# Kernel tuning notes

Hardware: AMD Instinct MI355X
Metric: run time of the kernel (lower is better)

The kernel has to match this reference:

```python
import jax, jax.numpy as jnp
import numpy as np

NEG_INF = jnp.float32(-9e15)

def gat_layer(x, adj_mask, W, a, alpha):
    # x: [N, F_in]; W: [H, F_in, F_out]; a: [H, 2*F_out]; adj_mask: [N, N] bool
    H, _, O = W.shape
    h = jnp.einsum('nf,hfo->hno', x, W)            # [H, N, O]
    a_src, a_dst = a[:, :O], a[:, O:]              # [H, O] each
    e_src = jnp.einsum('hno,ho->hn', h, a_src)     # [H, N]
    e_dst = jnp.einsum('hno,ho->hn', h, a_dst)     # [H, N]
    e = jax.nn.leaky_relu(e_src[:, :, None] + e_dst[:, None, :], negative_slope=alpha)
    e = jnp.where(adj_mask[None, :, :], e, NEG_INF)  # mask non-edges
    attn = jax.nn.softmax(e, axis=-1)              # [H, N, N]
    out = jnp.einsum('hnm,hmo->hno', attn, h)      # [H, N, O]
    return out.mean(axis=0)                        # average heads -> [N, O]

def setup_inputs() -> dict:
    key = jax.random.key(0)
    ks = jax.random.split(key, 6)
    N, F_IN, F_HID, F_CLS, H = 4096, 512, 256, 16, 4
    x = jax.random.normal(ks[0], (N, F_IN), dtype=jnp.float32)
    adj = jax.random.randint(ks[1], (N, N), 0, 2, dtype=jnp.int32)
    W1 = jax.random.normal(ks[2], (H, F_IN, F_HID), dtype=jnp.float32) * 0.05
    a1 = jax.random.normal(ks[3], (H, 2 * F_HID), dtype=jnp.float32) * 0.05
    W2 = jax.random.normal(ks[4], (1, F_HID, F_CLS), dtype=jnp.float32) * 0.05
    a2 = jax.random.normal(ks[5], (1, 2 * F_CLS), dtype=jnp.float32) * 0.05
    return {"x": x, "adj": adj, "W1": W1, "a1": a1, "W2": W2, "a2": a2}

def reference(x, adj, W1, a1, W2, a2):
    alpha = 0.2
    adj_mask = adj > 0
    h = jax.nn.relu(gat_layer(x, adj_mask, W1, a1, alpha))        # layer1 + ReLU
    out = gat_layer(h, adj_mask, W2, a2, alpha)                    # layer2
    return jax.nn.log_softmax(out, axis=1)                         # [N, nclass]
```

## Files before the change

### kernel.cpp

```cpp
#include <hip/hip_runtime.h>
#include <stdint.h>

#define N_NODES 4096
#define F_IN    512
#define F_HID   256
#define F_CLS   16
#define NHEAD   4
#define ALPHA   0.2f
#define LOG2E   1.4426950408889634f

typedef __attribute__((ext_vector_type(8))) short short8;
typedef __attribute__((ext_vector_type(4))) float f32x4;

__device__ __forceinline__ float bf2f(unsigned short h) {
    unsigned u = ((unsigned)h) << 16; float f; __builtin_memcpy(&f, &u, 4); return f;
}
__device__ __forceinline__ unsigned short f2bf(float f) {
    unsigned u; __builtin_memcpy(&u, &f, 4);
    u += 0x7fffu + ((u >> 16) & 1u);
    return (unsigned short)(u >> 16);
}
__device__ __forceinline__ float lo_bf(unsigned u) { u <<= 16;          float f; __builtin_memcpy(&f,&u,4); return f; }
__device__ __forceinline__ float hi_bf(unsigned u) { u &= 0xffff0000u;  float f; __builtin_memcpy(&f,&u,4); return f; }

__device__ __forceinline__ void async_cp16(void* lds, const void* g) {
    __builtin_amdgcn_global_load_lds(
        (const __attribute__((address_space(1))) unsigned int*)g,
        (__attribute__((address_space(3))) unsigned int*)lds,
        16, 0, 0);
}

__device__ __forceinline__ void pipe_barrier_vm2() {
    __builtin_amdgcn_sched_barrier(0);
    __builtin_amdgcn_s_waitcnt(0x0072);
    __builtin_amdgcn_s_barrier();
    __builtin_amdgcn_sched_barrier(0);
}
__device__ __forceinline__ void pipe_barrier_vm3() {
    __builtin_amdgcn_sched_barrier(0);
    __builtin_amdgcn_s_waitcnt(0x0073);
    __builtin_amdgcn_s_barrier();
    __builtin_amdgcn_sched_barrier(0);
}

#define PREP_BM_BLOCKS   16384
#define PREP_CV_BLOCKS   1296
#define PREP_Z_BLOCKS    4
__global__ __launch_bounds__(256) void k_prep(const int* __restrict__ adj,
                                              const float* __restrict__ x,
                                              const float* __restrict__ W1,
                                              const float* __restrict__ W2,
                                              unsigned long long* __restrict__ bm,
                                              unsigned short* __restrict__ xb,
                                              unsigned short* __restrict__ W1t,
                                              float* __restrict__ W2t,
                                              float* __restrict__ ez) {
    int b = blockIdx.x;
    if (b < PREP_BM_BLOCKS) {
        int wv = threadIdx.x >> 6, lane = threadIdx.x & 63;
        int idx0 = b * 1024 + wv * 256;
        const int* p = adj + idx0 + lane;
        unsigned long long m0 = __ballot(p[0]   > 0);
        unsigned long long m1 = __ballot(p[64]  > 0);
        unsigned long long m2 = __ballot(p[128] > 0);
        unsigned long long m3 = __ballot(p[192] > 0);
        if (lane == 0) {
            int w = idx0 >> 6;
            bm[w] = m0; bm[w+1] = m1; bm[w+2] = m2; bm[w+3] = m3;
        }
        return;
    }
    if (b < PREP_BM_BLOCKS + PREP_CV_BLOCKS) {
        int tid = (b - PREP_BM_BLOCKS) * 256 + threadIdx.x;
        const int NXV = (N_NODES * F_IN) / 8;
        const int NW1 = NHEAD * 64 * F_HID;
        if (tid < NXV) {
            float4 a = *(const float4*)&x[tid * 8];
            float4 c = *(const float4*)&x[tid * 8 + 4];
            uint4 w;
            w.x = (unsigned)f2bf(a.x) | ((unsigned)f2bf(a.y) << 16);
            w.y = (unsigned)f2bf(a.z) | ((unsigned)f2bf(a.w) << 16);
            w.z = (unsigned)f2bf(c.x) | ((unsigned)f2bf(c.y) << 16);
            w.w = (unsigned)f2bf(c.z) | ((unsigned)f2bf(c.w) << 16);
            *(uint4*)&xb[tid * 8] = w;
        } else if (tid < NXV + NW1) {
            int j = tid - NXV;
            int o = j & 255, f8 = (j >> 8) & 63, h = j >> 14;
            float v[8];
            #pragma unroll
            for (int k = 0; k < 8; ++k)
                v[k] = W1[(size_t)(h * F_IN + f8 * 8 + k) * F_HID + o];
            uint4 w;
            w.x = (unsigned)f2bf(v[0]) | ((unsigned)f2bf(v[1]) << 16);
            w.y = (unsigned)f2bf(v[2]) | ((unsigned)f2bf(v[3]) << 16);
            w.z = (unsigned)f2bf(v[4]) | ((unsigned)f2bf(v[5]) << 16);
            w.w = (unsigned)f2bf(v[6]) | ((unsigned)f2bf(v[7]) << 16);
            *(uint4*)&W1t[(size_t)(h * F_HID + o) * F_IN + f8 * 8] = w;
        } else {
            int j = tid - NXV - NW1;
            if (j < F_HID * F_CLS) {
                int o = j >> 4, c = j & 15;
                W2t[c * F_HID + o] = W2[j];
            }
        }
        return;
    }
    {
        int zb = b - PREP_BM_BLOCKS - PREP_CV_BLOCKS;
        float4* z4 = (float4*)ez;
        #pragma unroll
        for (int r = 0; r < 8; ++r)
            z4[zb * 2048 + r * 256 + threadIdx.x] = make_float4(0.f, 0.f, 0.f, 0.f);
    }
}

__global__ __launch_bounds__(256, 4) void k_gemm1(const unsigned short* __restrict__ xb,
                                                  const unsigned short* __restrict__ W1t,
                                                  const float* __restrict__ a1,
                                                  unsigned short* __restrict__ h1t,
                                                  float* __restrict__ es1,
                                                  float* __restrict__ ed1) {
    __shared__ unsigned short Sld[3][6144];
    const int t = threadIdx.x;
    const int lane = t & 63, wv = t >> 6, quad = lane >> 4, l15 = lane & 15;
    const int wn = wv & 1, wo = wv >> 1;
    const int n0 = blockIdx.x * 128;
    const int oo0 = blockIdx.y * 64;
    const int h = blockIdx.z;
    const int kl = (lane >> 4) * 8;

    const unsigned short* gs[3];
    int loff[3];
    #pragma unroll
    for (int s = 0; s < 3; ++s) {
        int c = wv * 3 + s;
        loff[s] = c * 512;
        gs[s] = (c < 8)
            ? (xb  + (size_t)(n0 + c * 16 + l15) * F_IN + kl)
            : (W1t + (size_t)(h * F_HID + oo0 + (c - 8) * 16 + l15) * F_IN + kl);
    }
    #pragma unroll
    for (int s = 0; s < 3; ++s) async_cp16(&Sld[0][loff[s]], gs[s]);
    #pragma unroll
    for (int s = 0; s < 3; ++s) async_cp16(&Sld[1][loff[s]], gs[s] + 32);

    f32x4 acc[4][2] = {};
    int cur = 0;
    for (int it = 0; it < 16; ++it) {
        pipe_barrier_vm3();
        {
            const int nxt = (cur >= 1) ? cur - 1 : 2;
            const int off = ((it + 2) & 15) * 32;
            #pragma unroll
            for (int s = 0; s < 3; ++s) async_cp16(&Sld[nxt][loff[s]], gs[s] + off);
        }
        short8 bfw[2];
        #pragma unroll
        for (int mi = 0; mi < 2; ++mi)
            bfw[mi] = *(const short8*)&Sld[cur][(8 + wo * 2 + mi) * 512 + lane * 8];
        #pragma unroll
        for (int ni = 0; ni < 4; ++ni) {
            short8 af = *(const short8*)&Sld[cur][(wn * 4 + ni) * 512 + lane * 8];
            #pragma unroll
            for (int mi = 0; mi < 2; ++mi)
                acc[ni][mi] = __builtin_amdgcn_mfma_f32_16x16x32_bf16(af, bfw[mi], acc[ni][mi], 0, 0, 0);
        }
        cur = (cur == 2) ? 0 : cur + 1;
    }
    #pragma unroll
    for (int ni = 0; ni < 4; ++ni)
      #pragma unroll
      for (int mi = 0; mi < 2; ++mi) {
        int o = oo0 + wo * 32 + mi * 16 + l15;
        int nb = n0 + wn * 64 + ni * 16 + quad * 4;
        uint2 uu;
        uu.x = (unsigned)f2bf(acc[ni][mi][0]) | ((unsigned)f2bf(acc[ni][mi][1]) << 16);
        uu.y = (unsigned)f2bf(acc[ni][mi][2]) | ((unsigned)f2bf(acc[ni][mi][3]) << 16);
        *(uint2*)&h1t[(size_t)(h * F_HID + o) * N_NODES + nb] = uu;
      }
    float a1s[2], a1d[2];
    #pragma unroll
    for (int mi = 0; mi < 2; ++mi) {
        int o = oo0 + wo * 32 + mi * 16 + l15;
        a1s[mi] = a1[h * 2 * F_HID + o] * LOG2E;
        a1d[mi] = a1[h * 2 * F_HID + F_HID + o] * LOG2E;
    }
    #pragma unroll
    for (int ni = 0; ni < 4; ++ni) {
        #pragma unroll
        for (int rg = 0; rg < 4; ++rg) {
            float es = acc[ni][0][rg] * a1s[0] + acc[ni][1][rg] * a1s[1];
            float ed = acc[ni][0][rg] * a1d[0] + acc[ni][1][rg] * a1d[1];
            #pragma unroll
            for (int off = 1; off < 16; off <<= 1) {
                es += __shfl_xor(es, off, 64);
                ed += __shfl_xor(ed, off, 64);
            }
            if (l15 == 0) {
                int n = n0 + wn * 64 + ni * 16 + quad * 4 + rg;
                atomicAdd(&es1[h * N_NODES + n], es);
                atomicAdd(&ed1[h * N_NODES + n], ed);
            }
        }
    }
}

__global__ __launch_bounds__(512, 2) void k_attn1(const unsigned short* __restrict__ h1t,
                                                  const float* __restrict__ es1,
                                                  const float* __restrict__ ed1,
                                                  const unsigned char* __restrict__ bmb,
                                                  unsigned short* __restrict__ C1p,
                                                  float* __restrict__ l1p) {
    __shared__ unsigned short Bld[3][8192];
    const int t = threadIdx.x;
    const int lane = t & 63, wv = t >> 6, quad = lane >> 4, l15 = lane & 15;
    const int m0 = blockIdx.x * 256;
    const int h = blockIdx.y;
    const int kz = blockIdx.z;
    const int mb0 = kz * 1024;

    const int m_r0 = m0 + wv * 32 + l15;
    const int m_r1 = m_r0 + 16;
    const float esr0 = es1[h * N_NODES + m_r0];
    const float esr1 = es1[h * N_NODES + m_r1];
    const unsigned char* bp0 = bmb + (size_t)m_r0 * (N_NODES / 8);
    const unsigned char* bp1 = bmb + (size_t)m_r1 * (N_NODES / 8);
    const float* edb = ed1 + h * N_NODES;

    const unsigned short* gb0 = h1t + (size_t)(h * F_HID + wv * 16 + l15) * N_NODES + (lane >> 4) * 8;
    const unsigned short* gb1 = h1t + (size_t)(h * F_HID + (wv + 8) * 16 + l15) * N_NODES + (lane >> 4) * 8;
    async_cp16(&Bld[0][wv * 512], gb0 + mb0);
    async_cp16(&Bld[0][(wv + 8) * 512], gb1 + mb0);
    async_cp16(&Bld[1][wv * 512], gb0 + mb0 + 32);
    async_cp16(&Bld[1][(wv + 8) * 512], gb1 + mb0 + 32);

    f32x4 acc[16][2] = {};
    float lsum0 = 0.f, lsum1 = 0.f;
    int cur = 0;
    for (int it = 0; it < 32; ++it) {
        const int mb = mb0 + it * 32;
        pipe_barrier_vm2();
        {
            const int nxt = (cur >= 1) ? cur - 1 : 2;
            const int mbp = mb0 + ((it + 2) & 31) * 32;
            async_cp16(&Bld[nxt][wv * 512], gb0 + mbp);
            async_cp16(&Bld[nxt][(wv + 8) * 512], gb1 + mbp);
        }
        float4 e0 = *(const float4*)&edb[mb + quad * 8];
        float4 e1v = *(const float4*)&edb[mb + quad * 8 + 4];
        float ev[8] = {e0.x, e0.y, e0.z, e0.w, e1v.x, e1v.y, e1v.z, e1v.w};
        unsigned bb0 = bp0[(mb >> 3) + quad];
        unsigned bb1 = bp1[(mb >> 3) + quad];
        unsigned up0[8], up1[8];
        #pragma unroll
        for (int j = 0; j < 8; ++j) {
            float s0 = esr0 + ev[j]; s0 = fmaxf(s0, ALPHA * s0);
            float p0 = ((bb0 >> j) & 1u) ? __builtin_amdgcn_exp2f(s0) : 0.f;
            unsigned u0; __builtin_memcpy(&u0, &p0, 4); u0 &= 0xffff0000u;
            float pt0; __builtin_memcpy(&pt0, &u0, 4);
            lsum0 += pt0; up0[j] = u0;
            float s1 = esr1 + ev[j]; s1 = fmaxf(s1, ALPHA * s1);
            float p1 = ((bb1 >> j) & 1u) ? __builtin_amdgcn_exp2f(s1) : 0.f;
            unsigned u1; __builtin_memcpy(&u1, &p1, 4); u1 &= 0xffff0000u;
            float pt1; __builtin_memcpy(&pt1, &u1, 4);
            lsum1 += pt1; up1[j] = u1;
        }
        int pk0[4], pk1[4];
        #pragma unroll
        for (int j = 0; j < 4; ++j) {
            pk0[j] = __builtin_amdgcn_perm(up0[2*j+1], up0[2*j], 0x07060302u);
            pk1[j] = __builtin_amdgcn_perm(up1[2*j+1], up1[2*j], 0x07060302u);
        }
        short8 bfrag0, bfrag1;
        __builtin_memcpy(&bfrag0, pk0, 16);
        __builtin_memcpy(&bfrag1, pk1, 16);
        #pragma unroll
        for (int ot = 0; ot < 16; ++ot) {
            short8 af = *(const short8*)&Bld[cur][ot * 512 + lane * 8];
            acc[ot][0] = __builtin_amdgcn_mfma_f32_16x16x32_bf16(af, bfrag0, acc[ot][0], 0, 0, 0);
            acc[ot][1] = __builtin_amdgcn_mfma_f32_16x16x32_bf16(af, bfrag1, acc[ot][1], 0, 0, 0);
        }
        cur = (cur == 2) ? 0 : cur + 1;
    }
    lsum0 += __shfl_xor(lsum0, 16, 64); lsum0 += __shfl_xor(lsum0, 32, 64);
    lsum1 += __shfl_xor(lsum1, 16, 64); lsum1 += __shfl_xor(lsum1, 32, 64);
    if (quad == 0) {
        l1p[(size_t)(kz * NHEAD + h) * N_NODES + m_r0] = lsum0;
        l1p[(size_t)(kz * NHEAD + h) * N_NODES + m_r1] = lsum1;
    }
    unsigned short* Cb = C1p + (size_t)(kz * NHEAD + h) * N_NODES * F_HID;
    #pragma unroll
    for (int ot = 0; ot < 16; ++ot)
      #pragma unroll
      for (int mi = 0; mi < 2; ++mi) {
        int m = (mi == 0) ? m_r0 : m_r1;
        int o0 = ot * 16 + quad * 4;
        uint2 uu;
        uu.x = (unsigned)f2bf(acc[ot][mi][0]) | ((unsigned)f2bf(acc[ot][mi][1]) << 16);
        uu.y = (unsigned)f2bf(acc[ot][mi][2]) | ((unsigned)f2bf(acc[ot][mi][3]) << 16);
        *(uint2*)&Cb[(size_t)m * F_HID + o0] = uu;
      }
}

__global__ __launch_bounds__(256) void k_reduce1(const unsigned short* __restrict__ C1p,
                                                 const float* __restrict__ l1p,
                                                 unsigned short* __restrict__ h2) {
    int t = threadIdx.x;
    int og = t & 31, nl = t >> 5;
    int n = blockIdx.x * 8 + nl;
    float acc8[8] = {};
    #pragma unroll
    for (int h = 0; h < NHEAD; ++h) {
        float den = 0.f, num[8] = {};
        #pragma unroll
        for (int kz = 0; kz < 4; ++kz) {
            den += l1p[(size_t)(kz * NHEAD + h) * N_NODES + n];
            uint4 u = *(const uint4*)&C1p[((size_t)(kz * NHEAD + h) * N_NODES + n) * F_HID + og * 8];
            num[0] += lo_bf(u.x); num[1] += hi_bf(u.x);
            num[2] += lo_bf(u.y); num[3] += hi_bf(u.y);
            num[4] += lo_bf(u.z); num[5] += hi_bf(u.z);
            num[6] += lo_bf(u.w); num[7] += hi_bf(u.w);
        }
        float rinv = 1.f / fmaxf(den, 1e-30f);
        #pragma unroll
        for (int j = 0; j < 8; ++j) acc8[j] += num[j] * rinv;
    }
    uint4 w;
    unsigned short bq[8];
    #pragma unroll
    for (int j = 0; j < 8; ++j) bq[j] = f2bf(fmaxf(acc8[j] * 0.25f, 0.f));
    w.x = (unsigned)bq[0] | ((unsigned)bq[1] << 16);
    w.y = (unsigned)bq[2] | ((unsigned)bq[3] << 16);
    w.z = (unsigned)bq[4] | ((unsigned)bq[5] << 16);
    w.w = (unsigned)bq[6] | ((unsigned)bq[7] << 16);
    *(uint4*)&h2[(size_t)n * F_HID + og * 8] = w;
}

__global__ __launch_bounds__(256) void k_h2w(const unsigned short* __restrict__ h2,
                                             const float* __restrict__ W2t,
                                             const float* __restrict__ a2,
                                             unsigned short* __restrict__ h2wt,
                                             float* __restrict__ es2, float* __restrict__ ed2) {
    int t = threadIdx.x;
    int c = t & 15, nl = t >> 4;
    int n = blockIdx.x * 16 + nl;
    const unsigned short* hrow = h2 + (size_t)n * F_HID;
    const float* wrow = W2t + c * F_HID;
    float dot = 0.f;
    for (int o = 0; o < F_HID; o += 8) {
        uint4 hu = *(const uint4*)&hrow[o];
        float4 w0 = *(const float4*)&wrow[o];
        float4 w1 = *(const float4*)&wrow[o + 4];
        dot += lo_bf(hu.x)*w0.x + hi_bf(hu.x)*w0.y + lo_bf(hu.y)*w0.z + hi_bf(hu.y)*w0.w;
        dot += lo_bf(hu.z)*w1.x + hi_bf(hu.z)*w1.y + lo_bf(hu.w)*w1.z + hi_bf(hu.w)*w1.w;
    }
    h2wt[(size_t)c * N_NODES + n] = f2bf(dot);
    float es = dot * a2[c] * LOG2E;
    float ed = dot * a2[F_CLS + c] * LOG2E;
    #pragma unroll
    for (int off = 1; off < 16; off <<= 1) {
        es += __shfl_xor(es, off, 64);
        ed += __shfl_xor(ed, off, 64);
    }
    if (c == 0) { es2[n] = es; ed2[n] = ed; }
}

__global__ __launch_bounds__(256, 4) void k_attn2(const unsigned short* __restrict__ h2wt,
                                                  const float* __restrict__ es2,
                                                  const float* __restrict__ ed2,
                                                  const unsigned char* __restrict__ bmb,
                                                  float* __restrict__ out2p,
                                                  float* __restrict__ l2p) {
    const int t = threadIdx.x;
    const int lane = t & 63, wv = t >> 6, quad = lane >> 4, l15 = lane & 15;
    const int m0 = blockIdx.x * 64;
    const int ks = blockIdx.y;
    const int m_r = m0 + wv * 16 + l15;
    const float esr = es2[m_r];
    const unsigned char* bp = bmb + (size_t)m_r * (N_NODES / 8);

    f32x4 acc = {};
    float lsum = 0.f;
    for (int it = 0; it < 16; ++it) {
        const int mb = ks * 512 + it * 32;
        float4 e0 = *(const float4*)&ed2[mb + quad * 8];
        float4 e1v = *(const float4*)&ed2[mb + quad * 8 + 4];
        float ev[8] = {e0.x, e0.y, e0.z, e0.w, e1v.x, e1v.y, e1v.z, e1v.w};
        unsigned bb = bp[(mb >> 3) + quad];
        short8 afrag;
        #pragma unroll
        for (int j = 0; j < 8; ++j) {
            float s = esr + ev[j]; s = fmaxf(s, ALPHA * s);
            float p = ((bb >> j) & 1u) ? __builtin_amdgcn_exp2f(s) : 0.f;
            lsum += p; afrag[j] = (short)f2bf(p);
        }
        short8 bfr = *(const short8*)&h2wt[(size_t)l15 * N_NODES + mb + quad * 8];
        acc = __builtin_amdgcn_mfma_f32_16x16x32_bf16(afrag, bfr, acc, 0, 0, 0);
    }
    lsum += __shfl_xor(lsum, 16, 64); lsum += __shfl_xor(lsum, 32, 64);
    if (quad == 0) l2p[(size_t)ks * N_NODES + m_r] = lsum;
    #pragma unroll
    for (int rg = 0; rg < 4; ++rg) {
        int row = m0 + wv * 16 + quad * 4 + rg;
        out2p[((size_t)ks * N_NODES + row) * F_CLS + l15] = acc[rg];
    }
}

__global__ __launch_bounds__(256) void k_final(const float* __restrict__ out2p,
                                               const float* __restrict__ l2p,
                                               float* __restrict__ out) {
    int t = threadIdx.x;
    int c = t & 15, nl = t >> 4;
    int n = blockIdx.x * 16 + nl;
    float v = 0.f, l = 0.f;
    #pragma unroll
    for (int ks = 0; ks < 8; ++ks) {
        v += out2p[((size_t)ks * N_NODES + n) * F_CLS + c];
        l += l2p[(size_t)ks * N_NODES + n];
    }
    v /= fmaxf(l, 1e-30f);
    float mx = v;
    #pragma unroll
    for (int off = 1; off < 16; off <<= 1) mx = fmaxf(mx, __shfl_xor(mx, off, 64));
    float e = __expf(v - mx);
    float se = e;
    #pragma unroll
    for (int off = 1; off < 16; off <<= 1) se += __shfl_xor(se, off, 64);
    out[(size_t)n * F_CLS + c] = v - mx - __logf(se);
}

#define OFF_BM    0ull
#define OFF_XB    2097152ull
#define OFF_W1T   6291456ull
#define OFF_W2T   7340032ull
#define OFF_ES1   7356416ull
#define OFF_ED1   7421952ull
#define OFF_ES2   7487488ull
#define OFF_ED2   7503872ull
#define OFF_L1P   7520256ull
#define OFF_L2P   7782400ull
#define OFF_H2    7910400ull
#define OFF_OUT2P 7910400ull
#define OFF_H2WT  10007552ull
#define OFF_H1T   10138624ull
#define OFF_C1P   18527232ull

extern "C" void kernel_launch(void* const* d_in, const int* in_sizes, int n_in,
                              void* d_out, int out_size, void* d_ws, size_t ws_size,
                              hipStream_t stream) {
    const float* x   = (const float*)d_in[0];
    const int*   adj = (const int*)d_in[1];
    const float* W1  = (const float*)d_in[2];
    const float* a1  = (const float*)d_in[3];
    const float* W2  = (const float*)d_in[4];
    const float* a2  = (const float*)d_in[5];
    float* out = (float*)d_out;
    char* ws = (char*)d_ws;

    unsigned long long* bm  = (unsigned long long*)(ws + OFF_BM);
    unsigned char*      bmb = (unsigned char*)(ws + OFF_BM);
    unsigned short* xb   = (unsigned short*)(ws + OFF_XB);
    unsigned short* W1t  = (unsigned short*)(ws + OFF_W1T);
    float* W2t   = (float*)(ws + OFF_W2T);
    float* es1   = (float*)(ws + OFF_ES1);
    float* ed1   = (float*)(ws + OFF_ED1);
    float* es2   = (float*)(ws + OFF_ES2);
    float* ed2   = (float*)(ws + OFF_ED2);
    float* l1p   = (float*)(ws + OFF_L1P);
    float* l2p   = (float*)(ws + OFF_L2P);
    unsigned short* h2   = (unsigned short*)(ws + OFF_H2);
    float* out2p = (float*)(ws + OFF_OUT2P);
    unsigned short* h2wt = (unsigned short*)(ws + OFF_H2WT);
    unsigned short* h1t  = (unsigned short*)(ws + OFF_H1T);
    unsigned short* C1p  = (unsigned short*)(ws + OFF_C1P);

    k_prep    <<<dim3(PREP_BM_BLOCKS + PREP_CV_BLOCKS + PREP_Z_BLOCKS), 256, 0, stream>>>(
                  adj, x, W1, W2, bm, xb, W1t, W2t, es1);
    k_gemm1   <<<dim3(32, 4, 4), 256, 0, stream>>>(xb, W1t, a1, h1t, es1, ed1);
    k_attn1   <<<dim3(16, 4, 4), 512, 0, stream>>>(h1t, es1, ed1, bmb, C1p, l1p);
    k_reduce1 <<<dim3(512),      256, 0, stream>>>(C1p, l1p, h2);
    k_h2w     <<<dim3(256),      256, 0, stream>>>(h2, W2t, a2, h2wt, es2, ed2);
    k_attn2   <<<dim3(64, 8),    256, 0, stream>>>(h2wt, es2, ed2, bmb, out2p, l2p);
    k_final   <<<dim3(256),      256, 0, stream>>>(out2p, l2p, out);
}
```

Before: 231.6 us.

## Retile attention kernel to smaller blocks and prefetch mask/edge data in registers

k_attn1 goes from 512-thread blocks over 256 rows to 256-thread blocks over 64 rows, with each wave pair splitting the 256 output features. The grid grows to 1024 blocks for better CU occupancy. Both attention kernels now load the adjacency bitmask 16 bytes at a time and software-prefetch the next edge scores and h2 fragments, which hides global load latency. The cost is that each block reloads the full h1t tile from LDS for only 64 rows, so the exp work per row is repeated by both wave halves and global traffic per output rises.

```diff
diff --git a/kernel.cpp b/kernel.cpp
--- a/kernel.cpp
+++ b/kernel.cpp
@@ -30,15 +30,15 @@
         16, 0, 0);
 }
 
-__device__ __forceinline__ void pipe_barrier_vm2() {
-    __builtin_amdgcn_sched_barrier(0);
-    __builtin_amdgcn_s_waitcnt(0x0072);
-    __builtin_amdgcn_s_barrier();
-    __builtin_amdgcn_sched_barrier(0);
-}
 __device__ __forceinline__ void pipe_barrier_vm3() {
     __builtin_amdgcn_sched_barrier(0);
     __builtin_amdgcn_s_waitcnt(0x0073);
+    __builtin_amdgcn_s_barrier();
+    __builtin_amdgcn_sched_barrier(0);
+}
+__device__ __forceinline__ void pipe_barrier_vm4() {
+    __builtin_amdgcn_sched_barrier(0);
+    __builtin_amdgcn_s_waitcnt(0x0074);
     __builtin_amdgcn_s_barrier();
     __builtin_amdgcn_sched_barrier(0);
 }
@@ -205,7 +205,7 @@
     }
 }
 
-__global__ __launch_bounds__(512, 2) void k_attn1(const unsigned short* __restrict__ h1t,
+__global__ __launch_bounds__(256, 3) void k_attn1(const unsigned short* __restrict__ h1t,
                                                   const float* __restrict__ es1,
                                                   const float* __restrict__ ed1,
                                                   const unsigned char* __restrict__ bmb,
@@ -214,87 +214,112 @@
     __shared__ unsigned short Bld[3][8192];
     const int t = threadIdx.x;
     const int lane = t & 63, wv = t >> 6, quad = lane >> 4, l15 = lane & 15;
-    const int m0 = blockIdx.x * 256;
+    const int wo = wv & 1, wm = wv >> 1;
+    const int m0 = blockIdx.x * 64;
     const int h = blockIdx.y;
     const int kz = blockIdx.z;
     const int mb0 = kz * 1024;
 
-    const int m_r0 = m0 + wv * 32 + l15;
+    const int m_r0 = m0 + wm * 32 + l15;
     const int m_r1 = m_r0 + 16;
     const float esr0 = es1[h * N_NODES + m_r0];
     const float esr1 = es1[h * N_NODES + m_r1];
-    const unsigned char* bp0 = bmb + (size_t)m_r0 * (N_NODES / 8);
-    const unsigned char* bp1 = bmb + (size_t)m_r1 * (N_NODES / 8);
-    const float* edb = ed1 + h * N_NODES;
-
-    const unsigned short* gb0 = h1t + (size_t)(h * F_HID + wv * 16 + l15) * N_NODES + (lane >> 4) * 8;
-    const unsigned short* gb1 = h1t + (size_t)(h * F_HID + (wv + 8) * 16 + l15) * N_NODES + (lane >> 4) * 8;
-    async_cp16(&Bld[0][wv * 512], gb0 + mb0);
-    async_cp16(&Bld[0][(wv + 8) * 512], gb1 + mb0);
-    async_cp16(&Bld[1][wv * 512], gb0 + mb0 + 32);
-    async_cp16(&Bld[1][(wv + 8) * 512], gb1 + mb0 + 32);
-
-    f32x4 acc[16][2] = {};
+    const unsigned char* bp0 = bmb + (size_t)m_r0 * (N_NODES / 8) + (mb0 >> 3);
+    const unsigned char* bp1 = bmb + (size_t)m_r1 * (N_NODES / 8) + (mb0 >> 3);
+    const float* edb = ed1 + h * N_NODES + mb0;
+
+    const unsigned short* gs[4];
+    int loff[4];
+    #pragma unroll
+    for (int s = 0; s < 4; ++s) {
+        int c = wv * 4 + s;
+        loff[s] = c * 512;
+        gs[s] = h1t + (size_t)(h * F_HID + c * 16 + l15) * N_NODES + mb0 + quad * 8;
+    }
+    #pragma unroll
+    for (int s = 0; s < 4; ++s) async_cp16(&Bld[0][loff[s]], gs[s]);
+    #pragma unroll
+    for (int s = 0; s < 4; ++s) async_cp16(&Bld[1][loff[s]], gs[s] + 32);
+
+    uint4 bq0 = *(const uint4*)bp0;
+    uint4 bq1 = *(const uint4*)bp1;
+    float4 e0 = *(const float4*)&edb[quad * 8];
+    float4 e1 = *(const float4*)&edb[quad * 8 + 4];
+
+    f32x4 acc[8][2] = {};
     float lsum0 = 0.f, lsum1 = 0.f;
     int cur = 0;
-    for (int it = 0; it < 32; ++it) {
-        const int mb = mb0 + it * 32;
-        pipe_barrier_vm2();
-        {
-            const int nxt = (cur >= 1) ? cur - 1 : 2;
-            const int mbp = mb0 + ((it + 2) & 31) * 32;
-            async_cp16(&Bld[nxt][wv * 512], gb0 + mbp);
-            async_cp16(&Bld[nxt][(wv + 8) * 512], gb1 + mbp);
-        }
-        float4 e0 = *(const float4*)&edb[mb + quad * 8];
-        float4 e1v = *(const float4*)&edb[mb + quad * 8 + 4];
-        float ev[8] = {e0.x, e0.y, e0.z, e0.w, e1v.x, e1v.y, e1v.z, e1v.w};
-        unsigned bb0 = bp0[(mb >> 3) + quad];
-        unsigned bb1 = bp1[(mb >> 3) + quad];
-        unsigned up0[8], up1[8];
-        #pragma unroll
-        for (int j = 0; j < 8; ++j) {
-            float s0 = esr0 + ev[j]; s0 = fmaxf(s0, ALPHA * s0);
-            float p0 = ((bb0 >> j) & 1u) ? __builtin_amdgcn_exp2f(s0) : 0.f;
-            unsigned u0; __builtin_memcpy(&u0, &p0, 4); u0 &= 0xffff0000u;
-            float pt0; __builtin_memcpy(&pt0, &u0, 4);
-            lsum0 += pt0; up0[j] = u0;
-            float s1 = esr1 + ev[j]; s1 = fmaxf(s1, ALPHA * s1);
-            float p1 = ((bb1 >> j) & 1u) ? __builtin_amdgcn_exp2f(s1) : 0.f;
-            unsigned u1; __builtin_memcpy(&u1, &p1, 4); u1 &= 0xffff0000u;
-            float pt1; __builtin_memcpy(&pt1, &u1, 4);
-            lsum1 += pt1; up1[j] = u1;
-        }
-        int pk0[4], pk1[4];
-        #pragma unroll
-        for (int j = 0; j < 4; ++j) {
-            pk0[j] = __builtin_amdgcn_perm(up0[2*j+1], up0[2*j], 0x07060302u);
-            pk1[j] = __builtin_amdgcn_perm(up1[2*j+1], up1[2*j], 0x07060302u);
-        }
-        short8 bfrag0, bfrag1;
-        __builtin_memcpy(&bfrag0, pk0, 16);
-        __builtin_memcpy(&bfrag1, pk1, 16);
-        #pragma unroll
-        for (int ot = 0; ot < 16; ++ot) {
-            short8 af = *(const short8*)&Bld[cur][ot * 512 + lane * 8];
-            acc[ot][0] = __builtin_amdgcn_mfma_f32_16x16x32_bf16(af, bfrag0, acc[ot][0], 0, 0, 0);
-            acc[ot][1] = __builtin_amdgcn_mfma_f32_16x16x32_bf16(af, bfrag1, acc[ot][1], 0, 0, 0);
-        }
-        cur = (cur == 2) ? 0 : cur + 1;
+    for (int it4 = 0; it4 < 8; ++it4) {
+        uint4 nbq0, nbq1;
+        #pragma unroll
+        for (int sub = 0; sub < 4; ++sub) {
+            const int it = it4 * 4 + sub;
+            pipe_barrier_vm4();
+            const int itn = (it + 1) & 31;
+            float4 ne0 = *(const float4*)&edb[itn * 32 + quad * 8];
+            float4 ne1 = *(const float4*)&edb[itn * 32 + quad * 8 + 4];
+            if (sub == 0) {
+                nbq0 = *(const uint4*)(bp0 + (it4 + 1) * 16);
+                nbq1 = *(const uint4*)(bp1 + (it4 + 1) * 16);
+            }
+            {
+                const int nxt = (cur >= 1) ? cur - 1 : 2;
+                const int mbp = ((it + 2) & 31) * 32;
+                #pragma unroll
+                for (int s = 0; s < 4; ++s) async_cp16(&Bld[nxt][loff[s]], gs[s] + mbp);
+            }
+            const unsigned d0[4] = {bq0.x, bq0.y, bq0.z, bq0.w};
+            const unsigned d1[4] = {bq1.x, bq1.y, bq1.z, bq1.w};
+            unsigned bb0 = (d0[sub] >> (quad * 8)) & 0xffu;
+            unsigned bb1 = (d1[sub] >> (quad * 8)) & 0xffu;
+            float ev[8] = {e0.x, e0.y, e0.z, e0.w, e1.x, e1.y, e1.z, e1.w};
+            unsigned up0[8], up1[8];
+            #pragma unroll
+            for (int j = 0; j < 8; ++j) {
+                float s0 = esr0 + ev[j]; s0 = fmaxf(s0, ALPHA * s0);
+                float p0 = ((bb0 >> j) & 1u) ? __builtin_amdgcn_exp2f(s0) : 0.f;
+                unsigned u0; __builtin_memcpy(&u0, &p0, 4); u0 &= 0xffff0000u;
+                float pt0; __builtin_memcpy(&pt0, &u0, 4);
+                lsum0 += pt0; up0[j] = u0;
+                float s1 = esr1 + ev[j]; s1 = fmaxf(s1, ALPHA * s1);
+                float p1 = ((bb1 >> j) & 1u) ? __builtin_amdgcn_exp2f(s1) : 0.f;
+                unsigned u1; __builtin_memcpy(&u1, &p1, 4); u1 &= 0xffff0000u;
+                float pt1; __builtin_memcpy(&pt1, &u1, 4);
+                lsum1 += pt1; up1[j] = u1;
+            }
+            int pk0[4], pk1[4];
+            #pragma unroll
+            for (int j = 0; j < 4; ++j) {
+                pk0[j] = __builtin_amdgcn_perm(up0[2*j+1], up0[2*j], 0x07060302u);
+                pk1[j] = __builtin_amdgcn_perm(up1[2*j+1], up1[2*j], 0x07060302u);
+            }
+            short8 bfrag0, bfrag1;
+            __builtin_memcpy(&bfrag0, pk0, 16);
+            __builtin_memcpy(&bfrag1, pk1, 16);
+            #pragma unroll
+            for (int ot = 0; ot < 8; ++ot) {
+                short8 af = *(const short8*)&Bld[cur][(wo * 8 + ot) * 512 + lane * 8];
+                acc[ot][0] = __builtin_amdgcn_mfma_f32_16x16x32_bf16(af, bfrag0, acc[ot][0], 0, 0, 0);
+                acc[ot][1] = __builtin_amdgcn_mfma_f32_16x16x32_bf16(af, bfrag1, acc[ot][1], 0, 0, 0);
+            }
+            e0 = ne0; e1 = ne1;
+            if (sub == 3) { bq0 = nbq0; bq1 = nbq1; }
+            cur = (cur == 2) ? 0 : cur + 1;
+        }
     }
     lsum0 += __shfl_xor(lsum0, 16, 64); lsum0 += __shfl_xor(lsum0, 32, 64);
     lsum1 += __shfl_xor(lsum1, 16, 64); lsum1 += __shfl_xor(lsum1, 32, 64);
-    if (quad == 0) {
+    if (quad == 0 && wo == 0) {
         l1p[(size_t)(kz * NHEAD + h) * N_NODES + m_r0] = lsum0;
         l1p[(size_t)(kz * NHEAD + h) * N_NODES + m_r1] = lsum1;
     }
     unsigned short* Cb = C1p + (size_t)(kz * NHEAD + h) * N_NODES * F_HID;
     #pragma unroll
-    for (int ot = 0; ot < 16; ++ot)
+    for (int ot = 0; ot < 8; ++ot)
       #pragma unroll
       for (int mi = 0; mi < 2; ++mi) {
         int m = (mi == 0) ? m_r0 : m_r1;
-        int o0 = ot * 16 + quad * 4;
+        int o0 = wo * 128 + ot * 16 + quad * 4;
         uint2 uu;
         uu.x = (unsigned)f2bf(acc[ot][mi][0]) | ((unsigned)f2bf(acc[ot][mi][1]) << 16);
         uu.y = (unsigned)f2bf(acc[ot][mi][2]) | ((unsigned)f2bf(acc[ot][mi][3]) << 16);
@@ -375,27 +400,44 @@
     const int lane = t & 63, wv = t >> 6, quad = lane >> 4, l15 = lane & 15;
     const int m0 = blockIdx.x * 64;
     const int ks = blockIdx.y;
+    const int mb0 = ks * 512;
     const int m_r = m0 + wv * 16 + l15;
     const float esr = es2[m_r];
-    const unsigned char* bp = bmb + (size_t)m_r * (N_NODES / 8);
+    const unsigned char* bp = bmb + (size_t)m_r * (N_NODES / 8) + (mb0 >> 3);
+    const float* edb = ed2 + mb0;
+    const unsigned short* hb = h2wt + (size_t)l15 * N_NODES + mb0 + quad * 8;
+
+    uint4 bq = *(const uint4*)bp;
+    float4 e0 = *(const float4*)&edb[quad * 8];
+    float4 e1 = *(const float4*)&edb[quad * 8 + 4];
+    short8 bfr = *(const short8*)&hb[0];
 
     f32x4 acc = {};
     float lsum = 0.f;
-    for (int it = 0; it < 16; ++it) {
-        const int mb = ks * 512 + it * 32;
-        float4 e0 = *(const float4*)&ed2[mb + quad * 8];
-        float4 e1v = *(const float4*)&ed2[mb + quad * 8 + 4];
-        float ev[8] = {e0.x, e0.y, e0.z, e0.w, e1v.x, e1v.y, e1v.z, e1v.w};
-        unsigned bb = bp[(mb >> 3) + quad];
-        short8 afrag;
-        #pragma unroll
-        for (int j = 0; j < 8; ++j) {
-            float s = esr + ev[j]; s = fmaxf(s, ALPHA * s);
-            float p = ((bb >> j) & 1u) ? __builtin_amdgcn_exp2f(s) : 0.f;
-            lsum += p; afrag[j] = (short)f2bf(p);
-        }
-        short8 bfr = *(const short8*)&h2wt[(size_t)l15 * N_NODES + mb + quad * 8];
-        acc = __builtin_amdgcn_mfma_f32_16x16x32_bf16(afrag, bfr, acc, 0, 0, 0);
+    for (int it4 = 0; it4 < 4; ++it4) {
+        uint4 nbq;
+        #pragma unroll
+        for (int sub = 0; sub < 4; ++sub) {
+            const int it = it4 * 4 + sub;
+            const int itn = (it + 1) & 15;
+            float4 ne0 = *(const float4*)&edb[itn * 32 + quad * 8];
+            float4 ne1 = *(const float4*)&edb[itn * 32 + quad * 8 + 4];
+            short8 nbf = *(const short8*)&hb[itn * 32];
+            if (sub == 0) nbq = *(const uint4*)(bp + (it4 + 1) * 16);
+            const unsigned d[4] = {bq.x, bq.y, bq.z, bq.w};
+            unsigned bb = (d[sub] >> (quad * 8)) & 0xffu;
+            float ev[8] = {e0.x, e0.y, e0.z, e0.w, e1.x, e1.y, e1.z, e1.w};
+            short8 afrag;
+            #pragma unroll
+            for (int j = 0; j < 8; ++j) {
+                float s = esr + ev[j]; s = fmaxf(s, ALPHA * s);
+                float p = ((bb >> j) & 1u) ? __builtin_amdgcn_exp2f(s) : 0.f;
+                lsum += p; afrag[j] = (short)f2bf(p);
+            }
+            acc = __builtin_amdgcn_mfma_f32_16x16x32_bf16(afrag, bfr, acc, 0, 0, 0);
+            e0 = ne0; e1 = ne1; bfr = nbf;
+            if (sub == 3) bq = nbq;
+        }
     }
     lsum += __shfl_xor(lsum, 16, 64); lsum += __shfl_xor(lsum, 32, 64);
     if (quad == 0) l2p[(size_t)ks * N_NODES + m_r] = lsum;
@@ -477,7 +519,7 @@
     k_prep    <<<dim3(PREP_BM_BLOCKS + PREP_CV_BLOCKS + PREP_Z_BLOCKS), 256, 0, stream>>>(
                   adj, x, W1, W2, bm, xb, W1t, W2t, es1);
     k_gemm1   <<<dim3(32, 4, 4), 256, 0, stream>>>(xb, W1t, a1, h1t, es1, ed1);
-    k_attn1   <<<dim3(16, 4, 4), 512, 0, stream>>>(h1t, es1, ed1, bmb, C1p, l1p);
+    k_attn1   <<<dim3(64, 4, 4), 256, 0, stream>>>(h1t, es1, ed1, bmb, C1p, l1p);
     k_reduce1 <<<dim3(512),      256, 0, stream>>>(C1p, l1p, h2);
     k_h2w     <<<dim3(256),      256, 0, stream>>>(h2, W2t, a2, h2wt, es2, ed2);
     k_attn2   <<<dim3(64, 8),    256, 0, stream>>>(h2wt, es2, ed2, bmb, out2p, l2p);
```

After: 597.2 us. 158% more time.

## Fuse layer-1 reduce with layer-2 projection and batch adjacency bitmask loads

Applied to the files above, without the earlier changes.

Merges the head/split reduction kernel with the h2·W2 projection kernel. The h2 row is staged in shared memory instead of being written to and reread from global memory, and one launch is removed. In the layer-1 attention loop, the adjacency bitmask is now read as a 16-byte vector covering four iterations and prefetched one group ahead, replacing per-iteration byte loads. In exchange, only half the threads do the projection dot products, and the prefetched mask adds register pressure to an already heavy MFMA kernel.

```diff
diff --git a/kernel.cpp b/kernel.cpp
--- a/kernel.cpp
+++ b/kernel.cpp
@@ -223,64 +223,79 @@
     const int m_r1 = m_r0 + 16;
     const float esr0 = es1[h * N_NODES + m_r0];
     const float esr1 = es1[h * N_NODES + m_r1];
-    const unsigned char* bp0 = bmb + (size_t)m_r0 * (N_NODES / 8);
-    const unsigned char* bp1 = bmb + (size_t)m_r1 * (N_NODES / 8);
-    const float* edb = ed1 + h * N_NODES;
-
-    const unsigned short* gb0 = h1t + (size_t)(h * F_HID + wv * 16 + l15) * N_NODES + (lane >> 4) * 8;
-    const unsigned short* gb1 = h1t + (size_t)(h * F_HID + (wv + 8) * 16 + l15) * N_NODES + (lane >> 4) * 8;
-    async_cp16(&Bld[0][wv * 512], gb0 + mb0);
-    async_cp16(&Bld[0][(wv + 8) * 512], gb1 + mb0);
-    async_cp16(&Bld[1][wv * 512], gb0 + mb0 + 32);
-    async_cp16(&Bld[1][(wv + 8) * 512], gb1 + mb0 + 32);
+    const unsigned char* bp0 = bmb + (size_t)m_r0 * (N_NODES / 8) + (mb0 >> 3);
+    const unsigned char* bp1 = bmb + (size_t)m_r1 * (N_NODES / 8) + (mb0 >> 3);
+    const float* edb = ed1 + h * N_NODES + mb0;
+
+    const unsigned short* gb0 = h1t + (size_t)(h * F_HID + wv * 16 + l15) * N_NODES + mb0 + quad * 8;
+    const unsigned short* gb1 = h1t + (size_t)(h * F_HID + (wv + 8) * 16 + l15) * N_NODES + mb0 + quad * 8;
+    async_cp16(&Bld[0][wv * 512], gb0);
+    async_cp16(&Bld[0][(wv + 8) * 512], gb1);
+    async_cp16(&Bld[1][wv * 512], gb0 + 32);
+    async_cp16(&Bld[1][(wv + 8) * 512], gb1 + 32);
+
+    uint4 bq0 = *(const uint4*)bp0;
+    uint4 bq1 = *(const uint4*)bp1;
 
     f32x4 acc[16][2] = {};
     float lsum0 = 0.f, lsum1 = 0.f;
     int cur = 0;
-    for (int it = 0; it < 32; ++it) {
-        const int mb = mb0 + it * 32;
-        pipe_barrier_vm2();
-        {
-            const int nxt = (cur >= 1) ? cur - 1 : 2;
-            const int mbp = mb0 + ((it + 2) & 31) * 32;
-            async_cp16(&Bld[nxt][wv * 512], gb0 + mbp);
-            async_cp16(&Bld[nxt][(wv + 8) * 512], gb1 + mbp);
-        }
-        float4 e0 = *(const float4*)&edb[mb + quad * 8];
-        float4 e1v = *(const float4*)&edb[mb + quad * 8 + 4];
-        float ev[8] = {e0.x, e0.y, e0.z, e0.w, e1v.x, e1v.y, e1v.z, e1v.w};
-        unsigned bb0 = bp0[(mb >> 3) + quad];
-        unsigned bb1 = bp1[(mb >> 3) + quad];
-        unsigned up0[8], up1[8];
-        #pragma unroll
-        for (int j = 0; j < 8; ++j) {
-            float s0 = esr0 + ev[j]; s0 = fmaxf(s0, ALPHA * s0);
-            float p0 = ((bb0 >> j) & 1u) ? __builtin_amdgcn_exp2f(s0) : 0.f;
-            unsigned u0; __builtin_memcpy(&u0, &p0, 4); u0 &= 0xffff0000u;
-            float pt0; __builtin_memcpy(&pt0, &u0, 4);
-            lsum0 += pt0; up0[j] = u0;
-            float s1 = esr1 + ev[j]; s1 = fmaxf(s1, ALPHA * s1);
-            float p1 = ((bb1 >> j) & 1u) ? __builtin_amdgcn_exp2f(s1) : 0.f;
-            unsigned u1; __builtin_memcpy(&u1, &p1, 4); u1 &= 0xffff0000u;
-            float pt1; __builtin_memcpy(&pt1, &u1, 4);
-            lsum1 += pt1; up1[j] = u1;
-        }
-        int pk0[4], pk1[4];
-        #pragma unroll
-        for (int j = 0; j < 4; ++j) {
-            pk0[j] = __builtin_amdgcn_perm(up0[2*j+1], up0[2*j], 0x07060302u);
-            pk1[j] = __builtin_amdgcn_perm(up1[2*j+1], up1[2*j], 0x07060302u);
-        }
-        short8 bfrag0, bfrag1;
-        __builtin_memcpy(&bfrag0, pk0, 16);
-        __builtin_memcpy(&bfrag1, pk1, 16);
-        #pragma unroll
-        for (int ot = 0; ot < 16; ++ot) {
-            short8 af = *(const short8*)&Bld[cur][ot * 512 + lane * 8];
-            acc[ot][0] = __builtin_amdgcn_mfma_f32_16x16x32_bf16(af, bfrag0, acc[ot][0], 0, 0, 0);
-            acc[ot][1] = __builtin_amdgcn_mfma_f32_16x16x32_bf16(af, bfrag1, acc[ot][1], 0, 0, 0);
-        }
-        cur = (cur == 2) ? 0 : cur + 1;
+    for (int it4 = 0; it4 < 8; ++it4) {
+        uint4 nbq0, nbq1;
+        #pragma unroll
+        for (int sub = 0; sub < 4; ++sub) {
+            const int it = it4 * 4 + sub;
+            const int mb = it * 32;
+            pipe_barrier_vm2();
+            if (sub == 0) {
+                nbq0 = *(const uint4*)(bp0 + ((it4 + 1) & 7) * 16);
+                nbq1 = *(const uint4*)(bp1 + ((it4 + 1) & 7) * 16);
+            }
+            {
+                const int nxt = (cur >= 1) ? cur - 1 : 2;
+                const int mbp = ((it + 2) & 31) * 32;
+                async_cp16(&Bld[nxt][wv * 512], gb0 + mbp);
+                async_cp16(&Bld[nxt][(wv + 8) * 512], gb1 + mbp);
+            }
+            float4 e0 = *(const float4*)&edb[mb + quad * 8];
+            float4 e1v = *(const float4*)&edb[mb + quad * 8 + 4];
+            float ev[8] = {e0.x, e0.y, e0.z, e0.w, e1v.x, e1v.y, e1v.z, e1v.w};
+            const unsigned d0[4] = {bq0.x, bq0.y, bq0.z, bq0.w};
+            const unsigned d1[4] = {bq1.x, bq1.y, bq1.z, bq1.w};
+            unsigned bb0 = (d0[sub] >> (quad * 8)) & 0xffu;
+            unsigned bb1 = (d1[sub] >> (quad * 8)) & 0xffu;
+            unsigned up0[8], up1[8];
+            #pragma unroll
+            for (int j = 0; j < 8; ++j) {
+                float s0 = esr0 + ev[j]; s0 = fmaxf(s0, ALPHA * s0);
+                float p0 = ((bb0 >> j) & 1u) ? __builtin_amdgcn_exp2f(s0) : 0.f;
+                unsigned u0; __builtin_memcpy(&u0, &p0, 4); u0 &= 0xffff0000u;
+                float pt0; __builtin_memcpy(&pt0, &u0, 4);
+                lsum0 += pt0; up0[j] = u0;
+                float s1 = esr1 + ev[j]; s1 = fmaxf(s1, ALPHA * s1);
+                float p1 = ((bb1 >> j) & 1u) ? __builtin_amdgcn_exp2f(s1) : 0.f;
+                unsigned u1; __builtin_memcpy(&u1, &p1, 4); u1 &= 0xffff0000u;
+                float pt1; __builtin_memcpy(&pt1, &u1, 4);
+                lsum1 += pt1; up1[j] = u1;
+            }
+            int pk0[4], pk1[4];
+            #pragma unroll
+            for (int j = 0; j < 4; ++j) {
+                pk0[j] = __builtin_amdgcn_perm(up0[2*j+1], up0[2*j], 0x07060302u);
+                pk1[j] = __builtin_amdgcn_perm(up1[2*j+1], up1[2*j], 0x07060302u);
+            }
+            short8 bfrag0, bfrag1;
+            __builtin_memcpy(&bfrag0, pk0, 16);
+            __builtin_memcpy(&bfrag1, pk1, 16);
+            #pragma unroll
+            for (int ot = 0; ot < 16; ++ot) {
+                short8 af = *(const short8*)&Bld[cur][ot * 512 + lane * 8];
+                acc[ot][0] = __builtin_amdgcn_mfma_f32_16x16x32_bf16(af, bfrag0, acc[ot][0], 0, 0, 0);
+                acc[ot][1] = __builtin_amdgcn_mfma_f32_16x16x32_bf16(af, bfrag1, acc[ot][1], 0, 0, 0);
+            }
+            if (sub == 3) { bq0 = nbq0; bq1 = nbq1; }
+            cur = (cur == 2) ? 0 : cur + 1;
+        }
     }
     lsum0 += __shfl_xor(lsum0, 16, 64); lsum0 += __shfl_xor(lsum0, 32, 64);
     lsum1 += __shfl_xor(lsum1, 16, 64); lsum1 += __shfl_xor(lsum1, 32, 64);
@@ -302,9 +317,14 @@
       }
 }
 
-__global__ __launch_bounds__(256) void k_reduce1(const unsigned short* __restrict__ C1p,
-                                                 const float* __restrict__ l1p,
-                                                 unsigned short* __restrict__ h2) {
+__global__ __launch_bounds__(256) void k_reduce_h2w(const unsigned short* __restrict__ C1p,
+                                                    const float* __restrict__ l1p,
+                                                    const float* __restrict__ W2t,
+                                                    const float* __restrict__ a2,
+                                                    unsigned short* __restrict__ h2wt,
+                                                    float* __restrict__ es2,
+                                                    float* __restrict__ ed2) {
+    __shared__ float h2s[8][256];
     int t = threadIdx.x;
     int og = t & 31, nl = t >> 5;
     int n = blockIdx.x * 8 + nl;
@@ -325,44 +345,37 @@
         #pragma unroll
         for (int j = 0; j < 8; ++j) acc8[j] += num[j] * rinv;
     }
-    uint4 w;
-    unsigned short bq[8];
-    #pragma unroll
-    for (int j = 0; j < 8; ++j) bq[j] = f2bf(fmaxf(acc8[j] * 0.25f, 0.f));
-    w.x = (unsigned)bq[0] | ((unsigned)bq[1] << 16);
-    w.y = (unsigned)bq[2] | ((unsigned)bq[3] << 16);
-    w.z = (unsigned)bq[4] | ((unsigned)bq[5] << 16);
-    w.w = (unsigned)bq[6] | ((unsigned)bq[7] << 16);
-    *(uint4*)&h2[(size_t)n * F_HID + og * 8] = w;
-}
-
-__global__ __launch_bounds__(256) void k_h2w(const unsigned short* __restrict__ h2,
-                                             const float* __restrict__ W2t,
-                                             const float* __restrict__ a2,
-                                             unsigned short* __restrict__ h2wt,
-                                             float* __restrict__ es2, float* __restrict__ ed2) {
-    int t = threadIdx.x;
-    int c = t & 15, nl = t >> 4;
-    int n = blockIdx.x * 16 + nl;
-    const unsigned short* hrow = h2 + (size_t)n * F_HID;
-    const float* wrow = W2t + c * F_HID;
-    float dot = 0.f;
-    for (int o = 0; o < F_HID; o += 8) {
-        uint4 hu = *(const uint4*)&hrow[o];
-        float4 w0 = *(const float4*)&wrow[o];
-        float4 w1 = *(const float4*)&wrow[o + 4];
-        dot += lo_bf(hu.x)*w0.x + hi_bf(hu.x)*w0.y + lo_bf(hu.y)*w0.z + hi_bf(hu.y)*w0.w;
-        dot += lo_bf(hu.z)*w1.x + hi_bf(hu.z)*w1.y + lo_bf(hu.w)*w1.z + hi_bf(hu.w)*w1.w;
-    }
-    h2wt[(size_t)c * N_NODES + n] = f2bf(dot);
-    float es = dot * a2[c] * LOG2E;
-    float ed = dot * a2[F_CLS + c] * LOG2E;
-    #pragma unroll
-    for (int off = 1; off < 16; off <<= 1) {
-        es += __shfl_xor(es, off, 64);
-        ed += __shfl_xor(ed, off, 64);
-    }
-    if (c == 0) { es2[n] = es; ed2[n] = ed; }
+    #pragma unroll
+    for (int j = 0; j < 8; ++j) {
+        float v = fmaxf(acc8[j] * 0.25f, 0.f);
+        h2s[nl][og * 8 + j] = bf2f(f2bf(v));
+    }
+    __syncthreads();
+    if (t < 128) {
+        int c = t & 15, n2l = t >> 4;
+        int n2 = blockIdx.x * 8 + n2l;
+        const float* wrow = W2t + c * F_HID;
+        const float* hrow = h2s[n2l];
+        float dot = 0.f;
+        #pragma unroll 4
+        for (int o = 0; o < F_HID; o += 8) {
+            float4 hv0 = *(const float4*)&hrow[o];
+            float4 hv1 = *(const float4*)&hrow[o + 4];
+            float4 w0 = *(const float4*)&wrow[o];
+            float4 w1 = *(const float4*)&wrow[o + 4];
+            dot += hv0.x*w0.x + hv0.y*w0.y + hv0.z*w0.z + hv0.w*w0.w;
+            dot += hv1.x*w1.x + hv1.y*w1.y + hv1.z*w1.z + hv1.w*w1.w;
+        }
+        h2wt[(size_t)c * N_NODES + n2] = f2bf(dot);
+        float es = dot * a2[c] * LOG2E;
+        float ed = dot * a2[F_CLS + c] * LOG2E;
+        #pragma unroll
+        for (int off = 1; off < 16; off <<= 1) {
+            es += __shfl_xor(es, off, 64);
+            ed += __shfl_xor(ed, off, 64);
+        }
+        if (c == 0) { es2[n2] = es; ed2[n2] = ed; }
+    }
 }
 
 __global__ __launch_bounds__(256, 4) void k_attn2(const unsigned short* __restrict__ h2wt,
@@ -439,7 +452,6 @@
 #define OFF_ED2   7503872ull
 #define OFF_L1P   7520256ull
 #define OFF_L2P   7782400ull
-#define OFF_H2    7910400ull
 #define OFF_OUT2P 7910400ull
 #define OFF_H2WT  10007552ull
 #define OFF_H1T   10138624ull
@@ -468,18 +480,16 @@
     float* ed2   = (float*)(ws + OFF_ED2);
     float* l1p   = (float*)(ws + OFF_L1P);
     float* l2p   = (float*)(ws + OFF_L2P);
-    unsigned short* h2   = (unsigned short*)(ws + OFF_H2);
     float* out2p = (float*)(ws + OFF_OUT2P);
     unsigned short* h2wt = (unsigned short*)(ws + OFF_H2WT);
     unsigned short* h1t  = (unsigned short*)(ws + OFF_H1T);
     unsigned short* C1p  = (unsigned short*)(ws + OFF_C1P);
 
-    k_prep    <<<dim3(PREP_BM_BLOCKS + PREP_CV_BLOCKS + PREP_Z_BLOCKS), 256, 0, stream>>>(
-                  adj, x, W1, W2, bm, xb, W1t, W2t, es1);
-    k_gemm1   <<<dim3(32, 4, 4), 256, 0, stream>>>(xb, W1t, a1, h1t, es1, ed1);
-    k_attn1   <<<dim3(16, 4, 4), 512, 0, stream>>>(h1t, es1, ed1, bmb, C1p, l1p);
-    k_reduce1 <<<dim3(512),      256, 0, stream>>>(C1p, l1p, h2);
-    k_h2w     <<<dim3(256),      256, 0, stream>>>(h2, W2t, a2, h2wt, es2, ed2);
-    k_attn2   <<<dim3(64, 8),    256, 0, stream>>>(h2wt, es2, ed2, bmb, out2p, l2p);
-    k_final   <<<dim3(256),      256, 0, stream>>>(out2p, l2p, out);
-}
+    k_prep       <<<dim3(PREP_BM_BLOCKS + PREP_CV_BLOCKS + PREP_Z_BLOCKS), 256, 0, stream>>>(
+                     adj, x, W1, W2, bm, xb, W1t, W2t, es1);
+    k_gemm1      <<<dim3(32, 4, 4), 256, 0, stream>>>(xb, W1t, a1, h1t, es1, ed1);
+    k_attn1      <<<dim3(16, 4, 4), 512, 0, stream>>>(h1t, es1, ed1, bmb, C1p, l1p);
+    k_reduce_h2w <<<dim3(512),      256, 0, stream>>>(C1p, l1p, W2t, a2, h2wt, es2, ed2);
+    k_attn2      <<<dim3(64, 8),    256, 0, stream>>>(h2wt, es2, ed2, bmb, out2p, l2p);
+    k_final      <<<dim3(256),      256, 0, stream>>>(out2p, l2p, out);
+}
```

After: 396.8 us. 71.3% more time.
